# Optimization experiments

Hardware: AMD Instinct MI355X
Metric: run time of the kernel (lower is better)

The kernel has to match this reference:

```python
import jax, jax.numpy as jnp
import numpy as np

B, N_IN, N_DET, N_ANCH, N_OUT = 2048, 1024, 512, 8, 256
N_CHAN = 1 << N_ANCH  # 256 LUT channels per detector (seq_len==1, concat product)


def setup_inputs() -> dict:
    key = jax.random.key(0)
    k1, k2, k3 = jax.random.split(key, 3)
    x = jax.random.normal(k1, (B, N_IN), dtype=jnp.float32)
    anchors = jax.random.randint(k2, (N_DET, N_ANCH), 0, N_IN, dtype=jnp.int32)
    weights = jax.random.uniform(k3, (N_DET, N_CHAN, N_OUT), dtype=jnp.float32)
    return {"x": x, "anchors": anchors, "weights": weights}


def reference(x, anchors, weights):
    # x: [B, N_IN] float activations; anchors: [D, A] int indices into inputs;
    # weights: [D, C, O] per-detector LUT table with C = 2**A channels.
    D, A = anchors.shape
    # Gather anchor activations and threshold to bits: [B, D, A]
    bits = (x[:, anchors] > 0.0).astype(jnp.int32)
    # Pack bits into a LUT channel index per (batch, detector): [B, D]
    pow2 = (jnp.int32(1) << jnp.arange(A, dtype=jnp.int32))
    idx = jnp.einsum('bda,a->bd', bits, pow2)
    # Gather the selected LUT row per detector and accumulate over detectors.
    det = jnp.arange(D, dtype=jnp.int32)[None, :]  # [1, D]
    gathered = weights[det, idx]  # [B, D, O]
    out = jnp.sum(gathered, axis=1)  # [B, O]
    return out
```

## Files before the change

### kernel.cpp

```cpp
#include <hip/hip_runtime.h>


typedef float f32x4 __attribute__((ext_vector_type(4)));

#define B_TOT   2048
#define N_IN    1024
#define N_DET   512
#define N_ANCH  8
#define N_OUT   256

#define DET_G   8
#define DPG     (N_DET/DET_G)
#define BT2     32
#define DET_BYTES 262144

#define IDX_BYTES   ((size_t)B_TOT * N_DET)
#define PART_BYTES  ((size_t)DET_G * B_TOT * N_OUT * sizeof(float))

__global__ __launch_bounds__(256) void lut_idx_kernel(
    const float* __restrict__ x,
    const int*   __restrict__ anchors,
    unsigned char* __restrict__ idx_out)
{
    __shared__ unsigned char bits[N_IN];
    const int b = blockIdx.x;
    const int t = threadIdx.x;

    const float4* xg = reinterpret_cast<const float4*>(x + (size_t)b * N_IN);
    float4 v = xg[t];
    bits[t * 4 + 0] = v.x > 0.0f;
    bits[t * 4 + 1] = v.y > 0.0f;
    bits[t * 4 + 2] = v.z > 0.0f;
    bits[t * 4 + 3] = v.w > 0.0f;
    __syncthreads();

    #pragma unroll
    for (int k = 0; k < N_DET / 256; ++k) {
        int d = t + k * 256;
        const int4* a4 = reinterpret_cast<const int4*>(anchors + d * N_ANCH);
        int4 a0 = a4[0];
        int4 a1 = a4[1];
        unsigned idx = 0;
        idx |= (unsigned)bits[a0.x];
        idx |= (unsigned)bits[a0.y] << 1;
        idx |= (unsigned)bits[a0.z] << 2;
        idx |= (unsigned)bits[a0.w] << 3;
        idx |= (unsigned)bits[a1.x] << 4;
        idx |= (unsigned)bits[a1.y] << 5;
        idx |= (unsigned)bits[a1.z] << 6;
        idx |= (unsigned)bits[a1.w] << 7;
        idx_out[(size_t)b * N_DET + d] = (unsigned char)idx;
    }
}

__global__ __launch_bounds__(256, 2) void lut_gather_kernel(
    const unsigned char* __restrict__ idx,
    const float* __restrict__ weights,
    float* __restrict__ partial)
{
    const int bid = blockIdx.x;
    const int g   = bid & (DET_G - 1);
    const int bc  = bid >> 3;
    const int b0  = bc * BT2;
    const int d0  = g * DPG;

    __shared__ unsigned char idx_s[DPG][BT2];

    const int t = threadIdx.x;
    {
        int r  = t >> 3;
        int cc = t & 7;
        uint2 v = *reinterpret_cast<const uint2*>(
            idx + (size_t)(b0 + r) * N_DET + d0 + cc * 8);
        unsigned char* bs = (unsigned char*)&v;
        #pragma unroll
        for (int i = 0; i < 8; ++i) idx_s[cc * 8 + i][r] = bs[i];
    }
    __syncthreads();

    const int wave = t >> 6;
    const int lane = t & 63;
    const int lane16 = lane * 16;

    f32x4 acc[8];
    #pragma unroll
    for (int j = 0; j < 8; ++j) acc[j] = (f32x4){0.f, 0.f, 0.f, 0.f};

    __amdgpu_buffer_rsrc_t rs = __builtin_amdgcn_make_buffer_rsrc(
        (void*)(reinterpret_cast<const char*>(weights) + (size_t)d0 * DET_BYTES),
        (short)0, (int)(DPG * DET_BYTES), 0x00020000);

    unsigned w0 = __builtin_amdgcn_readfirstlane(
        *reinterpret_cast<const unsigned*>(&idx_s[0][wave * 8]));
    unsigned w1 = __builtin_amdgcn_readfirstlane(
        *reinterpret_cast<const unsigned*>(&idx_s[0][wave * 8 + 4]));

    #pragma unroll 2
    for (int d = 0; d < DPG; ++d) {
        const unsigned lo = w0, hi = w1;
        if (d + 1 < DPG) {
            w0 = __builtin_amdgcn_readfirstlane(
                *reinterpret_cast<const unsigned*>(&idx_s[d + 1][wave * 8]));
            w1 = __builtin_amdgcn_readfirstlane(
                *reinterpret_cast<const unsigned*>(&idx_s[d + 1][wave * 8 + 4]));
        }
        const int db = d * DET_BYTES;
        f32x4 r[8];
        #pragma unroll
        for (int j = 0; j < 4; ++j) {
            auto rv = __builtin_amdgcn_raw_buffer_load_b128(
                rs, lane16, db + (int)(((lo >> (8 * j)) & 0xFFu) << 10), 1);
            r[j] = __builtin_bit_cast(f32x4, rv);
        }
        #pragma unroll
        for (int j = 0; j < 4; ++j) {
            auto rv = __builtin_amdgcn_raw_buffer_load_b128(
                rs, lane16, db + (int)(((hi >> (8 * j)) & 0xFFu) << 10), 1);
            r[4 + j] = __builtin_bit_cast(f32x4, rv);
        }
        #pragma unroll
        for (int j = 0; j < 8; ++j)
            acc[j] += r[j];
    }

    f32x4* P4 = reinterpret_cast<f32x4*>(partial);
    #pragma unroll
    for (int j = 0; j < 8; ++j) {
        size_t b = (size_t)b0 + wave * 8 + j;
        __builtin_nontemporal_store(acc[j],
            &P4[((size_t)g * B_TOT + b) * 64 + lane]);
    }
}

__global__ __launch_bounds__(256) void lut_reduce_kernel(
    const float* __restrict__ partial,
    float* __restrict__ out)
{
    const size_t i = (size_t)blockIdx.x * 256 + threadIdx.x;
    const f32x4* P4 = reinterpret_cast<const f32x4*>(partial);
    f32x4 s = (f32x4){0.f, 0.f, 0.f, 0.f};
    #pragma unroll
    for (int g = 0; g < DET_G; ++g) {
        f32x4 v = __builtin_nontemporal_load(&P4[(size_t)g * (B_TOT * 64) + i]);
        s += v;
    }
    reinterpret_cast<f32x4*>(out)[i] = s;
}

#define BT 4
__global__ __launch_bounds__(256) void lut_fused_kernel(
    const float* __restrict__ x,
    const int*   __restrict__ anchors,
    const float* __restrict__ weights,
    float*       __restrict__ out)
{
    __shared__ float x_s[BT][N_IN];
    __shared__ int   idx_s[BT][N_DET];
    const int tid = threadIdx.x;
    const int b0  = blockIdx.x * BT;
    {
        const float4* xg = reinterpret_cast<const float4*>(x + (size_t)b0 * N_IN);
        float4*       xs = reinterpret_cast<float4*>(&x_s[0][0]);
        #pragma unroll
        for (int k = 0; k < BT; ++k) xs[tid + k * 256] = xg[tid + k * 256];
    }
    __syncthreads();
    #pragma unroll
    for (int k = 0; k < (BT * N_DET) / 256; ++k) {
        int p  = tid + k * 256;
        int d  = p & (N_DET - 1);
        int bt = p >> 9;
        const int4* a4 = reinterpret_cast<const int4*>(anchors + d * N_ANCH);
        int4 a0 = a4[0];
        int4 a1 = a4[1];
        int idx = 0;
        idx |= (x_s[bt][a0.x] > 0.0f) ? 1   : 0;
        idx |= (x_s[bt][a0.y] > 0.0f) ? 2   : 0;
        idx |= (x_s[bt][a0.z] > 0.0f) ? 4   : 0;
        idx |= (x_s[bt][a0.w] > 0.0f) ? 8   : 0;
        idx |= (x_s[bt][a1.x] > 0.0f) ? 16  : 0;
        idx |= (x_s[bt][a1.y] > 0.0f) ? 32  : 0;
        idx |= (x_s[bt][a1.z] > 0.0f) ? 64  : 0;
        idx |= (x_s[bt][a1.w] > 0.0f) ? 128 : 0;
        idx_s[bt][d] = idx;
    }
    __syncthreads();
    const int wave = tid >> 6;
    const int lane = tid & 63;
    float4 acc = make_float4(0.0f, 0.0f, 0.0f, 0.0f);
    const float4* W4 = reinterpret_cast<const float4*>(weights);
    #pragma unroll 8
    for (int d = 0; d < N_DET; ++d) {
        int idx = idx_s[wave][d];
        size_t row = (size_t)(d << 8) + (size_t)idx;
        float4 w = W4[row * 64 + lane];
        acc.x += w.x; acc.y += w.y; acc.z += w.z; acc.w += w.w;
    }
    float4* out4 = reinterpret_cast<float4*>(out + (size_t)(b0 + wave) * N_OUT);
    out4[lane] = acc;
}

extern "C" void kernel_launch(void* const* d_in, const int* in_sizes, int n_in,
                              void* d_out, int out_size, void* d_ws, size_t ws_size,
                              hipStream_t stream) {
    const float* x       = (const float*)d_in[0];
    const int*   anchors = (const int*)  d_in[1];
    const float* weights = (const float*)d_in[2];
    float*       out     = (float*)d_out;

    if (ws_size >= IDX_BYTES + PART_BYTES) {
        unsigned char* idx_ws  = (unsigned char*)d_ws;
        float*         part_ws = (float*)((char*)d_ws + IDX_BYTES);

        lut_idx_kernel<<<dim3(B_TOT), dim3(256), 0, stream>>>(x, anchors, idx_ws);
        lut_gather_kernel<<<dim3((B_TOT / BT2) * DET_G), dim3(256), 0, stream>>>(
            idx_ws, weights, part_ws);
        lut_reduce_kernel<<<dim3(B_TOT * N_OUT / 4 / 256), dim3(256), 0, stream>>>(
            part_ws, out);
    } else {
        lut_fused_kernel<<<dim3(B_TOT / BT), dim3(256), 0, stream>>>(
            x, anchors, weights, out);
    }
}
```

Before: 62.06 us.

## Stage per-detector LUT slices in LDS as bf16 and gather from shared memory

Adds a gather kernel that streams each detector's LUT slice for a 64-output subset into double-buffered LDS and converts it to packed bf16. Threads then look up rows for 512 batch rows from shared memory instead of doing random global loads. Partial sums are kept for 16 detector groups and reduced by a templated reduce kernel. This trades random global gathers for dense streaming of the whole weight table per batch chunk, and it lowers accumulation precision to bf16 inputs.

```diff
diff --git a/kernel.cpp b/kernel.cpp
--- a/kernel.cpp
+++ b/kernel.cpp
@@ -8,14 +8,24 @@
 #define N_DET   512
 #define N_ANCH  8
 #define N_OUT   256
-
-#define DET_G   8
-#define DPG     (N_DET/DET_G)
-#define BT2     32
 #define DET_BYTES 262144
 
+#define NDG   16
+#define DGD   32
+#define NOS   4
+#define OSF   64
+#define BCH   512
+
 #define IDX_BYTES   ((size_t)B_TOT * N_DET)
-#define PART_BYTES  ((size_t)DET_G * B_TOT * N_OUT * sizeof(float))
+#define PART2_BYTES ((size_t)NDG * B_TOT * N_OUT * 4)
+
+#define DET_G 8
+#define DPG   (N_DET/DET_G)
+#define BT2   32
+#define PART_BYTES ((size_t)DET_G * B_TOT * N_OUT * 4)
+
+__device__ inline float bitf(unsigned u) { return __builtin_bit_cast(float, u); }
+__device__ inline unsigned fbit(float f) { return __builtin_bit_cast(unsigned, f); }
 
 __global__ __launch_bounds__(256) void lut_idx_kernel(
     const float* __restrict__ x,
@@ -53,6 +63,112 @@
     }
 }
 
+__global__ __launch_bounds__(512) void lut_gather2(
+    const unsigned char* __restrict__ idx,
+    const float* __restrict__ weights,
+    float* __restrict__ partial)
+{
+    __shared__ uint4 buf[2][2048];
+
+    const int bid   = blockIdx.x;
+    const int chunk = bid >> 6;
+    const int dg    = (bid >> 2) & 15;
+    const int os    = bid & 3;
+    const int b0    = chunk * BCH;
+    const int d0    = dg * DGD;
+    const int o0    = os * OSF;
+
+    const int t = threadIdx.x;
+    const int w = t >> 6;
+    const int l = t & 63;
+
+    __amdgpu_buffer_rsrc_t rs = __builtin_amdgcn_make_buffer_rsrc(
+        (void*)weights, (short)0, (int)((size_t)N_DET * DET_BYTES), 0x00020000);
+
+    const int c_st  = t >> 1;
+    const int h_st  = t & 1;
+    const int vbase = c_st * 1024 + o0 * 4 + h_st * 128;
+
+    f32x4 rr[8];
+    {
+        const int soff = d0 * DET_BYTES;
+        #pragma unroll
+        for (int i = 0; i < 8; ++i) {
+            auto rv = __builtin_amdgcn_raw_buffer_load_b128(rs, vbase + i * 16, soff, 1);
+            rr[i] = __builtin_bit_cast(f32x4, rv);
+        }
+    }
+
+    f32x4 accA[8], accB[8];
+    #pragma unroll
+    for (int k = 0; k < 8; ++k) { accA[k] = 0.f; accB[k] = 0.f; }
+
+    const int bb0  = w * 64 + (l >> 3);
+    const int mych = l & 7;
+
+    for (int d = 0; d < DGD; ++d) {
+        const int cur = d & 1;
+        #pragma unroll
+        for (int i = 0; i < 4; ++i) {
+            unsigned e0 = fbit(rr[2*i][0]), e1 = fbit(rr[2*i][1]);
+            unsigned e2 = fbit(rr[2*i][2]), e3 = fbit(rr[2*i][3]);
+            unsigned f0 = fbit(rr[2*i+1][0]), f1 = fbit(rr[2*i+1][1]);
+            unsigned f2 = fbit(rr[2*i+1][2]), f3 = fbit(rr[2*i+1][3]);
+            uint4 wv;
+            wv.x = (((e0 + 0x8000u) >> 16)) | ((e1 + 0x8000u) & 0xFFFF0000u);
+            wv.y = (((e2 + 0x8000u) >> 16)) | ((e3 + 0x8000u) & 0xFFFF0000u);
+            wv.z = (((f0 + 0x8000u) >> 16)) | ((f1 + 0x8000u) & 0xFFFF0000u);
+            wv.w = (((f2 + 0x8000u) >> 16)) | ((f3 + 0x8000u) & 0xFFFF0000u);
+            buf[cur][c_st * 8 + (((h_st * 4 + i) ^ (c_st & 7)))] = wv;
+        }
+        if (d + 1 < DGD) {
+            const int soff = (d0 + d + 1) * DET_BYTES;
+            #pragma unroll
+            for (int i = 0; i < 8; ++i) {
+                auto rv = __builtin_amdgcn_raw_buffer_load_b128(rs, vbase + i * 16, soff, 1);
+                rr[i] = __builtin_bit_cast(f32x4, rv);
+            }
+        }
+        __syncthreads();
+
+        #pragma unroll
+        for (int k = 0; k < 8; ++k) {
+            int b = b0 + bb0 + 8 * k;
+            unsigned c = idx[(size_t)b * N_DET + d0 + d];
+            uint4 v = buf[cur][c * 8 + (mych ^ (c & 7))];
+            accA[k][0] += bitf(v.x << 16); accA[k][1] += bitf(v.x & 0xFFFF0000u);
+            accA[k][2] += bitf(v.y << 16); accA[k][3] += bitf(v.y & 0xFFFF0000u);
+            accB[k][0] += bitf(v.z << 16); accB[k][1] += bitf(v.z & 0xFFFF0000u);
+            accB[k][2] += bitf(v.w << 16); accB[k][3] += bitf(v.w & 0xFFFF0000u);
+        }
+    }
+
+    f32x4* P4 = reinterpret_cast<f32x4*>(partial);
+    #pragma unroll
+    for (int k = 0; k < 8; ++k) {
+        int b = b0 + bb0 + 8 * k;
+        size_t off4 = (((size_t)dg * B_TOT + b) * N_OUT + o0 + mych * 8) >> 2;
+        __builtin_nontemporal_store(accA[k], &P4[off4]);
+        __builtin_nontemporal_store(accB[k], &P4[off4 + 1]);
+    }
+}
+
+template <int NG>
+__global__ __launch_bounds__(256) void lut_reduce_kernel(
+    const float* __restrict__ partial,
+    float* __restrict__ out)
+{
+    const size_t i = (size_t)blockIdx.x * 256 + threadIdx.x;
+    const f32x4* P4 = reinterpret_cast<const f32x4*>(partial);
+    f32x4 s = (f32x4){0.f, 0.f, 0.f, 0.f};
+    #pragma unroll
+    for (int g = 0; g < NG; ++g) {
+        f32x4 v = __builtin_nontemporal_load(&P4[(size_t)g * (B_TOT * 64) + i]);
+        s += v;
+    }
+    reinterpret_cast<f32x4*>(out)[i] = s;
+}
+
 __global__ __launch_bounds__(256, 2) void lut_gather_kernel(
     const unsigned char* __restrict__ idx,
     const float* __restrict__ weights,
@@ -130,21 +246,6 @@
         __builtin_nontemporal_store(acc[j],
             &P4[((size_t)g * B_TOT + b) * 64 + lane]);
     }
-}
-
-__global__ __launch_bounds__(256) void lut_reduce_kernel(
-    const float* __restrict__ partial,
-    float* __restrict__ out)
-{
-    const size_t i = (size_t)blockIdx.x * 256 + threadIdx.x;
-    const f32x4* P4 = reinterpret_cast<const f32x4*>(partial);
-    f32x4 s = (f32x4){0.f, 0.f, 0.f, 0.f};
-    #pragma unroll
-    for (int g = 0; g < DET_G; ++g) {
-        f32x4 v = __builtin_nontemporal_load(&P4[(size_t)g * (B_TOT * 64) + i]);
-        s += v;
-    }
-    reinterpret_cast<f32x4*>(out)[i] = s;
 }
 
 #define BT 4
@@ -208,14 +309,23 @@
     const float* weights = (const float*)d_in[2];
     float*       out     = (float*)d_out;
 
-    if (ws_size >= IDX_BYTES + PART_BYTES) {
+    if (ws_size >= IDX_BYTES + PART2_BYTES) {
+        unsigned char* idx_ws  = (unsigned char*)d_ws;
+        float*         part_ws = (float*)((char*)d_ws + IDX_BYTES);
+
+        lut_idx_kernel<<<dim3(B_TOT), dim3(256), 0, stream>>>(x, anchors, idx_ws);
+        lut_gather2<<<dim3(NDG * NOS * (B_TOT / BCH)), dim3(512), 0, stream>>>(
+            idx_ws, weights, part_ws);
+        lut_reduce_kernel<16><<<dim3(B_TOT * N_OUT / 4 / 256), dim3(256), 0, stream>>>(
+            part_ws, out);
+    } else if (ws_size >= IDX_BYTES + PART_BYTES) {
         unsigned char* idx_ws  = (unsigned char*)d_ws;
         float*         part_ws = (float*)((char*)d_ws + IDX_BYTES);
 
         lut_idx_kernel<<<dim3(B_TOT), dim3(256), 0, stream>>>(x, anchors, idx_ws);
         lut_gather_kernel<<<dim3((B_TOT / BT2) * DET_G), dim3(256), 0, stream>>>(
             idx_ws, weights, part_ws);
-        lut_reduce_kernel<<<dim3(B_TOT * N_OUT / 4 / 256), dim3(256), 0, stream>>>(
+        lut_reduce_kernel<8><<<dim3(B_TOT * N_OUT / 4 / 256), dim3(256), 0, stream>>>(
             part_ws, out);
     } else {
         lut_fused_kernel<<<dim3(B_TOT / BT), dim3(256), 0, stream>>>(
```

Result: slower. 142.2 us (+129.1%).
